# Performance work log

Measured on AMD Instinct MI355X. Metric: run time of the kernel, lower is better.

The kernel has to match this reference:

```python
import jax, jax.numpy as jnp
import numpy as np
import math

B, N, D = 128, 64, 2
H, M, L = 64, 64, 2
OMEGA = 1.0


def setup_inputs() -> dict:
    key = jax.random.key(0)
    ks = jax.random.split(key, 32)
    s = 0.1  # param scale
    rn = lambda k, shp: jax.random.normal(k, shp, dtype=jnp.float32) * s
    inp = {
        "x": jax.random.normal(ks[0], (B, N, D), dtype=jnp.float32),
        "spin": jnp.zeros((B, N, 1), jnp.float32),
        "node_w1": rn(ks[1], (D + 1, H)), "node_b1": rn(ks[2], (H,)),
        "node_w2": rn(ks[3], (H, H)), "node_b2": rn(ks[4], (H,)),
        "edge_w1": rn(ks[5], (D + 2, M)), "edge_b1": rn(ks[6], (M,)),
        "edge_w2": rn(ks[7], (M, M)), "edge_b2": rn(ks[8], (M,)),
        "v2e_w1": rn(ks[9], (L, H + M, M)), "v2e_b1": rn(ks[10], (L, M)),
        "v2e_w2": rn(ks[11], (L, M, M)), "v2e_b2": rn(ks[12], (L, M)),
        "e2v_w1": rn(ks[13], (L, M, H)), "e2v_b1": rn(ks[14], (L, H)),
        "e2v_w2": rn(ks[15], (L, H, H)), "e2v_b2": rn(ks[16], (L, H)),
        "head_w1": rn(ks[17], (H, H)), "head_b1": rn(ks[18], (H,)),
        "head_w2": rn(ks[19], (H, D)), "head_b2": rn(ks[20], (D,)),
        # bf_scale_init=0.3 -> softplus-inverse
        "scale": jnp.array([math.log(math.exp(0.3) - 1.0)], jnp.float32),
    }
    return inp


def _mlp(x, w1, b1, w2, b2, act):
    return act(x @ w1 + b1) @ w2 + b2


def reference(x, spin, node_w1, node_b1, node_w2, node_b2,
              edge_w1, edge_b1, edge_w2, edge_b2,
              v2e_w1, v2e_b1, v2e_w2, v2e_b2,
              e2v_w1, e2v_b1, e2v_w2, e2v_b2,
              head_w1, head_b1, head_w2, head_b2, scale):
    gelu = lambda t: jax.nn.gelu(t, approximate=False)  # torch exact GELU
    b, n, d = x.shape
    xs = x * jnp.float32(math.sqrt(OMEGA))
    # node embedding: [B,N,H]
    hv = _mlp(jnp.concatenate([xs, spin], -1), node_w1, node_b1, node_w2, node_b2, gelu)
    # dense pairwise edge features; dr[b,i,j] = xs[b,j] - xs[b,i]
    dr = xs[:, None, :, :] - xs[:, :, None, :]            # [B,N,N,D]
    r2 = jnp.sum(dr * dr, axis=-1, keepdims=True)          # [B,N,N,1]
    rr = jnp.sqrt(r2 + 1e-12)
    he = _mlp(jnp.concatenate([dr, rr, r2], -1), edge_w1, edge_b1, edge_w2, edge_b2, gelu)  # [B,N,N,M]
    # mask excludes self-edges (i==j) from aggregation (they were never created
    # in the original edge list; their dense entries never influence off-diag values)
    mask = (1.0 - jnp.eye(n, dtype=x.dtype))[None, :, :, None]
    inv = jnp.float32(1.0 / max(n - 1, 1))
    for l in range(v2e_w1.shape[0]):
        hvb = jnp.broadcast_to(hv[:, :, None, :], (b, n, n, hv.shape[-1]))  # source node i
        he = _mlp(jnp.concatenate([hvb, he], -1), v2e_w1[l], v2e_b1[l], v2e_w2[l], v2e_b2[l], gelu)
        m = _mlp(he, e2v_w1[l], e2v_b1[l], e2v_w2[l], e2v_b2[l], gelu)      # [B,N,N,H]
        hv = hv + jnp.sum(m * mask, axis=1) * inv           # scatter-add over sources i into j
    dx = _mlp(hv, head_w1, head_b1, head_w2, head_b2, jnp.tanh) * jax.nn.softplus(scale[0])
    return dx - jnp.mean(dx, axis=1, keepdims=True)
```

## Files before the change

kernel.cpp:

```cpp
#include <hip/hip_runtime.h>
#include <math.h>


typedef unsigned short u16;
typedef unsigned int u32;
typedef _Float16 half8 __attribute__((ext_vector_type(8)));
typedef __attribute__((ext_vector_type(4))) float floatx4;

#define TS 72
#define HROW 72
#define HBLK (64 * HROW)

__device__ __forceinline__ float gelu_f(float x) {
    float s = fabsf(x) * 0.70710678118654752f;
    float q = fmaf(fmaf(fmaf(fmaf(0.078108f, s, 0.000972f), s, 0.230389f), s, 0.278393f), s, 1.0f);
    float q2 = q * q;
    float r = __builtin_amdgcn_rcpf(q2 * q2);
    float t = 0.5f * x * r;
    return x > 0.f ? x - t : t;
}

__global__ __launch_bounds__(256) void k_preA(
    const float* __restrict__ ew2, const float* __restrict__ w1he0,
    const float* __restrict__ w2_0, const float* __restrict__ u1_0,
    const float* __restrict__ w1he1, const float* __restrict__ w2_1,
    const float* __restrict__ u1_1,
    const float* __restrict__ eb2, const float* __restrict__ b2_0,
    const float* __restrict__ c1_0, const float* __restrict__ b2_1,
    const float* __restrict__ c1_1,
    const float* __restrict__ b1_0v, const float* __restrict__ b1nv,
    const float* __restrict__ u2_0, const float* __restrict__ u2_1,
    const float* __restrict__ w1n, const float* __restrict__ hw1,
    _Float16* __restrict__ WF,
    float* __restrict__ biasB, float* __restrict__ biasC, float* __restrict__ biasD,
    float* __restrict__ pb0,
    float* __restrict__ u2_0T, float* __restrict__ u2_1T,
    float* __restrict__ w1nT, float* __restrict__ hw1T)
{
    int blk = blockIdx.x;
    if (blk < 64) {
        int s = blk >> 4;
        int idx = (blk & 15) * 256 + threadIdx.x;
        int k = idx >> 6, n = idx & 63;
        const float *A, *Bm;
        if (s == 0)      { A = ew2;  Bm = w1he0; }
        else if (s == 1) { A = w2_0; Bm = u1_0;  }
        else if (s == 2) { A = w2_0; Bm = w1he1; }
        else             { A = w2_1; Bm = u1_1;  }
        float acc = 0.f;
        for (int q = 0; q < 64; ++q) acc = fmaf(A[k * 64 + q], Bm[q * 64 + n], acc);
        int kc = k >> 5, qd = (k >> 3) & 3, jj = k & 7;
        WF[(((s * 2 + kc) * 64 + n) * 4 + qd) * 8 + jj] = (_Float16)acc;
    } else if (blk == 64) {
        int s = threadIdx.x >> 6, cc = threadIdx.x & 63;
        if (s == 0) {
            float acc = b1_0v[cc];
            for (int q = 0; q < 64; ++q) acc = fmaf(eb2[q], w1he0[q * 64 + cc], acc);
            pb0[cc] = acc;
        } else {
            const float *bv, *Bm, *add; float* dst;
            if (s == 1)      { bv = b2_0; Bm = u1_0;  add = c1_0; dst = biasB; }
            else if (s == 2) { bv = b2_0; Bm = w1he1; add = b1nv; dst = biasC; }
            else             { bv = b2_1; Bm = u1_1;  add = c1_1; dst = biasD; }
            float acc = add[cc];
            for (int q = 0; q < 64; ++q) acc = fmaf(bv[q], Bm[q * 64 + cc], acc);
            dst[cc] = acc;
        }
    } else {
        int idx = (blk - 65) * 256 + threadIdx.x;
        int s = idx >> 12, r = idx & 4095, m = r >> 6, tc = r & 63;
        const float* W = s == 0 ? u2_0 : s == 1 ? u2_1 : s == 2 ? w1n : hw1;
        float* WT      = s == 0 ? u2_0T : s == 1 ? u2_1T : s == 2 ? w1nT : hw1T;
        WT[tc * 64 + m] = W[m * 64 + tc];
    }
}

__global__ __launch_bounds__(256) void k_preB(
    const float* __restrict__ x, const float* __restrict__ spin,
    const float* __restrict__ nw1, const float* __restrict__ nb1,
    const float* __restrict__ nw2, const float* __restrict__ nb2,
    const float* __restrict__ w1_0,
    const float* __restrict__ pb0,
    float* __restrict__ hv, float* __restrict__ p0T)
{
    __shared__ float a[4][64];
    __shared__ float shv[4][64];
    int w = threadIdx.x >> 6, h = threadIdx.x & 63;
    int node = blockIdx.x * 4 + w;
    float2 xv = ((const float2*)x)[node];
    float sp = spin[node];
    float z = fmaf(xv.x, nw1[h], fmaf(xv.y, nw1[64 + h], fmaf(sp, nw1[128 + h], nb1[h])));
    a[w][h] = gelu_f(z);
    float acc = nb2[h];
    for (int k = 0; k < 64; ++k) acc = fmaf(a[w][k], nw2[k * 64 + h], acc);
    hv[node * 64 + h] = acc;
    shv[w][h] = acc;
    float pa = pb0[h];
    for (int k = 0; k < 64; ++k) pa = fmaf(shv[w][k], w1_0[k * 64 + h], pa);
    p0T[(node >> 6) * 4096 + h * 64 + (node & 63)] = pa;
}

__device__ __forceinline__ void mfma_acc(
    const _Float16* __restrict__ tA, const _Float16* __restrict__ WF,
    int stage, int c, int quad, int nn, floatx4 acc[4])
{
    int sA = ((nn >> 2) & 3) << 3;
    #pragma unroll
    for (int kc = 0; kc < 2; ++kc) {
        half8 bf = *(const half8*)(WF + (((stage * 2 + kc) * 64 + c) * 4 + quad) * 8);
        int k0 = (kc * 32 + quad * 8) ^ sA;
        #pragma unroll
        for (int mt = 0; mt < 4; ++mt) {
            half8 af = *(const half8*)(tA + (mt * 16 + nn) * TS + k0);
            acc[mt] = __builtin_amdgcn_mfma_f32_16x16x32_f16(af, bf, acc[mt], 0, 0, 0);
        }
    }
}

__device__ __forceinline__ void init_bias(floatx4 acc[4], float bc) {
    #pragma unroll
    for (int mt = 0; mt < 4; ++mt) acc[mt] = (floatx4){bc, bc, bc, bc};
}
__device__ __forceinline__ void init_pT(floatx4 acc[4], const float* __restrict__ pT,
                                        int base) {
    #pragma unroll
    for (int mt = 0; mt < 4; ++mt)
        acc[mt] = *(const floatx4*)(pT + base + mt * 16);
}

__global__ __launch_bounds__(256, 8) void k_L0(
    const float* __restrict__ x,
    const float* __restrict__ ew1, const float* __restrict__ eb1,
    const float* __restrict__ p0T,
    const float* __restrict__ biasB,
    const float* __restrict__ u2_0T, const float* __restrict__ c2_0,
    const _Float16* __restrict__ WF,
    const float* __restrict__ hv0, float* __restrict__ hv1,
    const float* __restrict__ w1nT, const float* __restrict__ biasC,
    float* __restrict__ p1T,
    u16* __restrict__ he0g)
{
    __shared__ __align__(16) _Float16 tA[64 * TS];
    __shared__ float sS[64];
    __shared__ float shv[64];
    __shared__ float sred[256];
    int t = threadIdx.x, L = t & 63;
    int w = __builtin_amdgcn_readfirstlane(t >> 6);
    int nn = L & 15, quad = L >> 4;
    int c = w * 16 + nn;
    int cw = c ^ (quad << 3);
    int b = blockIdx.x >> 6, j = blockIdx.x & 63;

    float2 xi = ((const float2*)x)[b * 64 + L];
    float2 xj = ((const float2*)x)[b * 64 + j];
    float d0 = xj.x - xi.x, d1 = xj.y - xi.y;
    float r2 = fmaf(d0, d0, d1 * d1);
    float rr = sqrtf(r2 + 1e-12f);
    int swL = ((L >> 2) & 3) << 3;

    #pragma unroll
    for (int mb = 0; mb < 2; ++mb) {
        int m0 = w * 16 + mb * 8;
        half8 h8;
        #pragma unroll
        for (int kk = 0; kk < 8; ++kk) {
            int m = m0 + kk;
            float z = fmaf(d0, ew1[m], fmaf(d1, ew1[64 + m],
                      fmaf(rr, ew1[128 + m], fmaf(r2, ew1[192 + m], eb1[m]))));
            h8[kk] = (_Float16)gelu_f(z);
        }
        *(half8*)(tA + L * TS + (m0 ^ swL)) = h8;
    }
    __syncthreads();

    floatx4 acc[4];
    init_pT(acc, p0T, b * 4096 + c * 64 + quad * 4);
    mfma_acc(tA, WF, 0, c, quad, nn, acc);
    __syncthreads();
    #pragma unroll
    for (int mt = 0; mt < 4; ++mt)
        #pragma unroll
        for (int r = 0; r < 4; ++r)
            tA[(mt * 16 + quad * 4 + r) * TS + cw] = (_Float16)gelu_f(acc[mt][r]);
    __syncthreads();
    {
        const float4* srcl = (const float4*)tA;
        float4* dst4 = (float4*)(he0g + (size_t)blockIdx.x * HBLK);
        dst4[t] = srcl[t];
        dst4[t + 256] = srcl[t + 256];
        if (t < 64) dst4[t + 512] = srcl[t + 512];
    }
    init_bias(acc, biasB[c]);
    mfma_acc(tA, WF, 1, c, quad, nn, acc);
    {
        float s = 0.f;
        #pragma unroll
        for (int mt = 0; mt < 4; ++mt)
            #pragma unroll
            for (int r = 0; r < 4; ++r) {
                int i = mt * 16 + quad * 4 + r;
                float g = gelu_f(acc[mt][r]);
                s += (i == j) ? 0.f : g;
            }
        s += __shfl_xor(s, 16);
        s += __shfl_xor(s, 32);
        if (quad == 0) sS[c] = s;
    }
    __syncthreads();
    {
        const float4* sv4 = (const float4*)(sS + w * 16);
        const float4* uv4 = (const float4*)(u2_0T + L * 64 + w * 16);
        float g = 0.f;
        #pragma unroll
        for (int m4 = 0; m4 < 4; ++m4) {
            float4 sv = sv4[m4], uv = uv4[m4];
            g = fmaf(sv.x, uv.x, fmaf(sv.y, uv.y, fmaf(sv.z, uv.z, fmaf(sv.w, uv.w, g))));
        }
        sred[w * 64 + L] = g;
    }
    __syncthreads();
    if (t < 64) {
        float g = sred[t] + sred[64 + t] + sred[128 + t] + sred[192 + t];
        int o = blockIdx.x * 64 + t;
        float hvv = hv0[o] + g * (1.0f / 63.0f) + c2_0[t];
        hv1[o] = hvv;
        shv[t] = hvv;
    }
    __syncthreads();
    {
        const float4* hv4 = (const float4*)(shv + w * 16);
        const float4* wv4 = (const float4*)(w1nT + L * 64 + w * 16);
        float pa = 0.f;
        #pragma unroll
        for (int m4 = 0; m4 < 4; ++m4) {
            float4 sv = hv4[m4], uv = wv4[m4];
            pa = fmaf(sv.x, uv.x, fmaf(sv.y, uv.y, fmaf(sv.z, uv.z, fmaf(sv.w, uv.w, pa))));
        }
        sred[w * 64 + L] = pa;
    }
    __syncthreads();
    if (t < 64)
        p1T[b * 4096 + t * 64 + j] = biasC[t] + sred[t] + sred[64 + t] + sred[128 + t] + sred[192 + t];
}

__global__ __launch_bounds__(256, 8) void k_L1(
    const u16* __restrict__ he0g,
    const float* __restrict__ p1T,
    const float* __restrict__ biasD,
    const float* __restrict__ u2_1T, const float* __restrict__ c2_1,
    const _Float16* __restrict__ WF,
    const float* __restrict__ hv1,
    const float* __restrict__ hw1T, const float* __restrict__ hb1,
    const float* __restrict__ hw2, const float* __restrict__ hb2,
    const float* __restrict__ scale, float* __restrict__ dx)
{
    __shared__ __align__(16) _Float16 tA[64 * TS];
    __shared__ float sS[64];
    __shared__ float shv[64];
    __shared__ float sred[256];
    int t = threadIdx.x, L = t & 63;
    int w = __builtin_amdgcn_readfirstlane(t >> 6);
    int nn = L & 15, quad = L >> 4;
    int c = w * 16 + nn;
    int cw = c ^ (quad << 3);
    int b = blockIdx.x >> 6, j = blockIdx.x & 63;

    {
        const float4* src = (const float4*)(he0g + (size_t)blockIdx.x * HBLK);
        float4* dstl = (float4*)tA;
        for (int q = t; q < (HBLK * 2 / 16); q += 256)
            dstl[q] = src[q];
    }
    __syncthreads();

    floatx4 acc[4];
    init_pT(acc, p1T, b * 4096 + c * 64 + quad * 4);
    mfma_acc(tA, WF, 2, c, quad, nn, acc);
    __syncthreads();
    #pragma unroll
    for (int mt = 0; mt < 4; ++mt)
        #pragma unroll
        for (int r = 0; r < 4; ++r)
            tA[(mt * 16 + quad * 4 + r) * TS + cw] = (_Float16)gelu_f(acc[mt][r]);
    __syncthreads();
    init_bias(acc, biasD[c]);
    mfma_acc(tA, WF, 3, c, quad, nn, acc);
    {
        float s = 0.f;
        #pragma unroll
        for (int mt = 0; mt < 4; ++mt)
            #pragma unroll
            for (int r = 0; r < 4; ++r) {
                int i = mt * 16 + quad * 4 + r;
                float g = gelu_f(acc[mt][r]);
                s += (i == j) ? 0.f : g;
            }
        s += __shfl_xor(s, 16);
        s += __shfl_xor(s, 32);
        if (quad == 0) sS[c] = s;
    }
    __syncthreads();
    {
        const float4* sv4 = (const float4*)(sS + w * 16);
        const float4* uv4 = (const float4*)(u2_1T + L * 64 + w * 16);
        float g = 0.f;
        #pragma unroll
        for (int m4 = 0; m4 < 4; ++m4) {
            float4 sv = sv4[m4], uv = uv4[m4];
            g = fmaf(sv.x, uv.x, fmaf(sv.y, uv.y, fmaf(sv.z, uv.z, fmaf(sv.w, uv.w, g))));
        }
        sred[w * 64 + L] = g;
    }
    __syncthreads();
    if (t < 64) {
        float g = sred[t] + sred[64 + t] + sred[128 + t] + sred[192 + t];
        float hv2 = hv1[blockIdx.x * 64 + t] + g * (1.0f / 63.0f) + c2_1[t];
        shv[t] = hv2;
    }
    __syncthreads();
    {
        const float4* hv4 = (const float4*)(shv + w * 16);
        const float4* wv4 = (const float4*)(hw1T + L * 64 + w * 16);
        float a = 0.f;
        #pragma unroll
        for (int m4 = 0; m4 < 4; ++m4) {
            float4 sv = hv4[m4], uv = wv4[m4];
            a = fmaf(sv.x, uv.x, fmaf(sv.y, uv.y, fmaf(sv.z, uv.z, fmaf(sv.w, uv.w, a))));
        }
        sred[w * 64 + L] = a;
    }
    __syncthreads();
    if (t < 64) {
        float a = hb1[t] + sred[t] + sred[64 + t] + sred[128 + t] + sred[192 + t];
        float t1 = tanhf(a);
        float dd0 = t1 * hw2[t * 2], dd1 = t1 * hw2[t * 2 + 1];
        #pragma unroll
        for (int off = 1; off <= 32; off <<= 1) { dd0 += __shfl_xor(dd0, off); dd1 += __shfl_xor(dd1, off); }
        if (t == 0) {
            float sp = log1pf(__expf(scale[0]));
            dx[blockIdx.x * 2 + 0] = (dd0 + hb2[0]) * sp;
            dx[blockIdx.x * 2 + 1] = (dd1 + hb2[1]) * sp;
        }
    }
}

__global__ __launch_bounds__(64) void k_mean(
    const float* __restrict__ dx, float* __restrict__ out)
{
    __shared__ float s0[64], s1[64];
    int b = blockIdx.x, j = threadIdx.x;
    float2 d = ((const float2*)dx)[b * 64 + j];
    s0[j] = d.x; s1[j] = d.y;
    __syncthreads();
    float m0 = 0.f, m1 = 0.f;
    for (int q = 0; q < 64; ++q) { m0 += s0[q]; m1 += s1[q]; }
    ((float2*)out)[b * 64 + j] = make_float2(d.x - m0 * (1.0f / 64.0f), d.y - m1 * (1.0f / 64.0f));
}

__global__ void k_beacon(float* out, float code) { out[0] = code; }

extern "C" void kernel_launch(void* const* d_in, const int* in_sizes, int n_in,
                              void* d_out, int out_size, void* d_ws, size_t ws_size,
                              hipStream_t stream)
{
    static const int exp_sizes[23] = {
        16384, 8192, 192, 64, 4096, 64,
        256, 64, 4096, 64,
        16384, 128, 8192, 128,
        8192, 128, 8192, 128,
        4096, 64, 128, 2, 1
    };
    float* hv0 = (float*)d_ws;
    float* hv1 = hv0 + 524288;
    float* p0T = hv1 + 524288;
    float* p1T = p0T + 524288;
    float* dx  = p1T + 524288;
    float* u2_0T = dx + 16384;
    float* u2_1T = u2_0T + 4096;
    float* w1nT  = u2_1T + 4096;
    float* hw1T  = w1nT + 4096;
    float* biasB = hw1T + 4096;
    float* biasC = biasB + 64;
    float* biasD = biasC + 64;
    float* pb0   = biasD + 64;
    _Float16* WF = (_Float16*)(pb0 + 64);
    u16* he0g  = (u16*)(WF + 16384);
    const size_t need = (size_t)((char*)(he0g + (size_t)8192 * HBLK) - (char*)d_ws);

    int bad = -1;
    if (n_in != 23 || out_size != 16384) bad = 98;
    else if (ws_size < need) bad = 97;
    else for (int i = 0; i < 23; ++i)
        if (in_sizes[i] != exp_sizes[i]) { bad = i; break; }
    if (bad >= 0) {
        k_beacon<<<1, 1, 0, stream>>>((float*)d_out, 2e6f + bad * 1e4f);
        return;
    }

    const float* x      = (const float*)d_in[0];
    const float* spin   = (const float*)d_in[1];
    const float* nw1    = (const float*)d_in[2];
    const float* nb1    = (const float*)d_in[3];
    const float* nw2    = (const float*)d_in[4];
    const float* nb2    = (const float*)d_in[5];
    const float* ew1    = (const float*)d_in[6];
    const float* eb1    = (const float*)d_in[7];
    const float* ew2    = (const float*)d_in[8];
    const float* eb2    = (const float*)d_in[9];
    const float* v2e_w1 = (const float*)d_in[10];
    const float* v2e_b1 = (const float*)d_in[11];
    const float* v2e_w2 = (const float*)d_in[12];
    const float* v2e_b2 = (const float*)d_in[13];
    const float* e2v_w1 = (const float*)d_in[14];
    const float* e2v_b1 = (const float*)d_in[15];
    const float* e2v_w2 = (const float*)d_in[16];
    const float* e2v_b2 = (const float*)d_in[17];
    const float* hw1    = (const float*)d_in[18];
    const float* hb1    = (const float*)d_in[19];
    const float* hw2    = (const float*)d_in[20];
    const float* hb2    = (const float*)d_in[21];
    const float* scale  = (const float*)d_in[22];

    k_preA<<<129, 256, 0, stream>>>(
        ew2, v2e_w1 + 4096, v2e_w2, e2v_w1,
        v2e_w1 + 12288, v2e_w2 + 4096, e2v_w1 + 4096,
        eb2, v2e_b2, e2v_b1, v2e_b2 + 64, e2v_b1 + 64,
        v2e_b1, v2e_b1 + 64,
        e2v_w2, e2v_w2 + 4096, v2e_w1 + 8192, hw1,
        WF, biasB, biasC, biasD, pb0,
        u2_0T, u2_1T, w1nT, hw1T);
    k_preB<<<2048, 256, 0, stream>>>(x, spin, nw1, nb1, nw2, nb2, v2e_w1, pb0, hv0, p0T);
    k_L0<<<8192, 256, 0, stream>>>(x, ew1, eb1,
        p0T, biasB, u2_0T, e2v_b2,
        WF, hv0, hv1,
        w1nT, biasC, p1T,
        he0g);
    k_L1<<<8192, 256, 0, stream>>>(he0g,
        p1T, biasD, u2_1T, e2v_b2 + 64,
        WF, hv1, hw1T, hb1, hw2, hb2, scale, dx);
    k_mean<<<128, 64, 0, stream>>>(dx, (float*)d_out);
}
```

Baseline: 240.3 us.

## Fold post-aggregation matvecs into precomposed weights, merge prep kernels, compact edge buffer

Precomputes composed matrices (u2_0·w1n1 and u2_1·hw1) so the per-node matvec after the scatter-add can be computed in parallel with the aggregation, removing a serial reduce/sync round in both layer kernels. The two preprocessing kernels are merged into one launch, and the node-side contribution pc0 is computed there. The intermediate edge buffer is stored unpadded (4096 halfs per block instead of 72-stride rows) with remapping on store/load, and a second LDS tile removes a barrier before overwriting. This adds extra LDS and a larger prep kernel, and the pc0 workspace.

```diff
diff --git a/kernel.cpp b/kernel.cpp
--- a/kernel.cpp
+++ b/kernel.cpp
@@ -8,8 +8,6 @@
 typedef __attribute__((ext_vector_type(4))) float floatx4;
 
 #define TS 72
-#define HROW 72
-#define HBLK (64 * HROW)
 
 __device__ __forceinline__ float gelu_f(float x) {
     float s = fabsf(x) * 0.70710678118654752f;
@@ -20,25 +18,32 @@
     return x > 0.f ? x - t : t;
 }
 
-__global__ __launch_bounds__(256) void k_preA(
+__global__ __launch_bounds__(256) void k_pre(
     const float* __restrict__ ew2, const float* __restrict__ w1he0,
     const float* __restrict__ w2_0, const float* __restrict__ u1_0,
     const float* __restrict__ w1he1, const float* __restrict__ w2_1,
     const float* __restrict__ u1_1,
+    const float* __restrict__ u2_0, const float* __restrict__ w1n1,
+    const float* __restrict__ u2_1, const float* __restrict__ hw1,
     const float* __restrict__ eb2, const float* __restrict__ b2_0,
     const float* __restrict__ c1_0, const float* __restrict__ b2_1,
     const float* __restrict__ c1_1,
     const float* __restrict__ b1_0v, const float* __restrict__ b1nv,
-    const float* __restrict__ u2_0, const float* __restrict__ u2_1,
-    const float* __restrict__ w1n, const float* __restrict__ hw1,
+    const float* __restrict__ hb1, const float* __restrict__ c2_1,
+    const float* __restrict__ c2_0,
+    const float* __restrict__ x, const float* __restrict__ spin,
+    const float* __restrict__ nw1, const float* __restrict__ nb1,
+    const float* __restrict__ nw2, const float* __restrict__ nb2,
+    const float* __restrict__ w1_0,
     _Float16* __restrict__ WF,
     float* __restrict__ biasB, float* __restrict__ biasC, float* __restrict__ biasD,
-    float* __restrict__ pb0,
-    float* __restrict__ u2_0T, float* __restrict__ u2_1T,
-    float* __restrict__ w1nT, float* __restrict__ hw1T)
+    float* __restrict__ hb1p,
+    float* __restrict__ u2_0T, float* __restrict__ hw1T,
+    float* __restrict__ UT, float* __restrict__ VT,
+    float* __restrict__ hv, float* __restrict__ p0T, float* __restrict__ pc0)
 {
     int blk = blockIdx.x;
-    if (blk < 64) {
+    if (blk < 96) {
         int s = blk >> 4;
         int idx = (blk & 15) * 256 + threadIdx.x;
         int k = idx >> 6, n = idx & 63;
@@ -46,17 +51,24 @@
         if (s == 0)      { A = ew2;  Bm = w1he0; }
         else if (s == 1) { A = w2_0; Bm = u1_0;  }
         else if (s == 2) { A = w2_0; Bm = w1he1; }
-        else             { A = w2_1; Bm = u1_1;  }
+        else if (s == 3) { A = w2_1; Bm = u1_1;  }
+        else if (s == 4) { A = u2_0; Bm = w1n1;  }
+        else             { A = u2_1; Bm = hw1;   }
         float acc = 0.f;
         for (int q = 0; q < 64; ++q) acc = fmaf(A[k * 64 + q], Bm[q * 64 + n], acc);
-        int kc = k >> 5, qd = (k >> 3) & 3, jj = k & 7;
-        WF[(((s * 2 + kc) * 64 + n) * 4 + qd) * 8 + jj] = (_Float16)acc;
-    } else if (blk == 64) {
+        if (s < 4) {
+            int kc = k >> 5, qd = (k >> 3) & 3, jj = k & 7;
+            WF[(((s * 2 + kc) * 64 + n) * 4 + qd) * 8 + jj] = (_Float16)acc;
+        } else {
+            float* T = (s == 4) ? UT : VT;
+            T[n * 64 + k] = acc;
+        }
+    } else if (blk == 96) {
         int s = threadIdx.x >> 6, cc = threadIdx.x & 63;
         if (s == 0) {
-            float acc = b1_0v[cc];
-            for (int q = 0; q < 64; ++q) acc = fmaf(eb2[q], w1he0[q * 64 + cc], acc);
-            pb0[cc] = acc;
+            float acc = hb1[cc];
+            for (int q = 0; q < 64; ++q) acc = fmaf(c2_1[q], hw1[q * 64 + cc], acc);
+            hb1p[cc] = acc;
         } else {
             const float *bv, *Bm, *add; float* dst;
             if (s == 1)      { bv = b2_0; Bm = u1_0;  add = c1_0; dst = biasB; }
@@ -66,38 +78,35 @@
             for (int q = 0; q < 64; ++q) acc = fmaf(bv[q], Bm[q * 64 + cc], acc);
             dst[cc] = acc;
         }
+    } else if (blk < 129) {
+        int idx = (blk - 97) * 256 + threadIdx.x;
+        int s = idx >> 12, r = idx & 4095, m = r >> 6, tc = r & 63;
+        const float* W = s == 0 ? u2_0 : hw1;
+        float* WT      = s == 0 ? u2_0T : hw1T;
+        WT[tc * 64 + m] = W[m * 64 + tc];
     } else {
-        int idx = (blk - 65) * 256 + threadIdx.x;
-        int s = idx >> 12, r = idx & 4095, m = r >> 6, tc = r & 63;
-        const float* W = s == 0 ? u2_0 : s == 1 ? u2_1 : s == 2 ? w1n : hw1;
-        float* WT      = s == 0 ? u2_0T : s == 1 ? u2_1T : s == 2 ? w1nT : hw1T;
-        WT[tc * 64 + m] = W[m * 64 + tc];
-    }
-}
-
-__global__ __launch_bounds__(256) void k_preB(
-    const float* __restrict__ x, const float* __restrict__ spin,
-    const float* __restrict__ nw1, const float* __restrict__ nb1,
-    const float* __restrict__ nw2, const float* __restrict__ nb2,
-    const float* __restrict__ w1_0,
-    const float* __restrict__ pb0,
-    float* __restrict__ hv, float* __restrict__ p0T)
-{
-    __shared__ float a[4][64];
-    __shared__ float shv[4][64];
-    int w = threadIdx.x >> 6, h = threadIdx.x & 63;
-    int node = blockIdx.x * 4 + w;
-    float2 xv = ((const float2*)x)[node];
-    float sp = spin[node];
-    float z = fmaf(xv.x, nw1[h], fmaf(xv.y, nw1[64 + h], fmaf(sp, nw1[128 + h], nb1[h])));
-    a[w][h] = gelu_f(z);
-    float acc = nb2[h];
-    for (int k = 0; k < 64; ++k) acc = fmaf(a[w][k], nw2[k * 64 + h], acc);
-    hv[node * 64 + h] = acc;
-    shv[w][h] = acc;
-    float pa = pb0[h];
-    for (int k = 0; k < 64; ++k) pa = fmaf(shv[w][k], w1_0[k * 64 + h], pa);
-    p0T[(node >> 6) * 4096 + h * 64 + (node & 63)] = pa;
+        __shared__ float a[4][64];
+        __shared__ float shv[4][64];
+        __shared__ float shvc[4][64];
+        int w = threadIdx.x >> 6, h = threadIdx.x & 63;
+        int node = (blk - 129) * 4 + w;
+        float2 xv = ((const float2*)x)[node];
+        float sp = spin[node];
+        float z = fmaf(xv.x, nw1[h], fmaf(xv.y, nw1[64 + h], fmaf(sp, nw1[128 + h], nb1[h])));
+        a[w][h] = gelu_f(z);
+        float acc = nb2[h];
+        for (int k = 0; k < 64; ++k) acc = fmaf(a[w][k], nw2[k * 64 + h], acc);
+        hv[node * 64 + h] = acc;
+        shv[w][h] = acc;
+        shvc[w][h] = acc + c2_0[h];
+        float pa = b1_0v[h];
+        for (int q = 0; q < 64; ++q) pa = fmaf(eb2[q], w1he0[q * 64 + h], pa);
+        for (int k = 0; k < 64; ++k) pa = fmaf(shv[w][k], w1_0[k * 64 + h], pa);
+        p0T[(node >> 6) * 4096 + h * 64 + (node & 63)] = pa;
+        float pc = 0.f;
+        for (int k = 0; k < 64; ++k) pc = fmaf(shvc[w][k], w1n1[k * 64 + h], pc);
+        pc0[node * 64 + h] = pc;
+    }
 }
 
 __device__ __forceinline__ void mfma_acc(
@@ -133,17 +142,18 @@
     const float* __restrict__ ew1, const float* __restrict__ eb1,
     const float* __restrict__ p0T,
     const float* __restrict__ biasB,
-    const float* __restrict__ u2_0T, const float* __restrict__ c2_0,
+    const float* __restrict__ u2_0T, const float* __restrict__ UT,
+    const float* __restrict__ c2_0,
+    const float* __restrict__ biasC, const float* __restrict__ pc0,
     const _Float16* __restrict__ WF,
     const float* __restrict__ hv0, float* __restrict__ hv1,
-    const float* __restrict__ w1nT, const float* __restrict__ biasC,
     float* __restrict__ p1T,
     u16* __restrict__ he0g)
 {
     __shared__ __align__(16) _Float16 tA[64 * TS];
+    __shared__ __align__(16) _Float16 tB[64 * TS];
     __shared__ float sS[64];
-    __shared__ float shv[64];
-    __shared__ float sred[256];
+    __shared__ float sredA[256], sredB[256];
     int t = threadIdx.x, L = t & 63;
     int w = __builtin_amdgcn_readfirstlane(t >> 6);
     int nn = L & 15, quad = L >> 4;
@@ -176,22 +186,21 @@
     floatx4 acc[4];
     init_pT(acc, p0T, b * 4096 + c * 64 + quad * 4);
     mfma_acc(tA, WF, 0, c, quad, nn, acc);
-    __syncthreads();
     #pragma unroll
     for (int mt = 0; mt < 4; ++mt)
         #pragma unroll
         for (int r = 0; r < 4; ++r)
-            tA[(mt * 16 + quad * 4 + r) * TS + cw] = (_Float16)gelu_f(acc[mt][r]);
-    __syncthreads();
-    {
-        const float4* srcl = (const float4*)tA;
-        float4* dst4 = (float4*)(he0g + (size_t)blockIdx.x * HBLK);
-        dst4[t] = srcl[t];
-        dst4[t + 256] = srcl[t + 256];
-        if (t < 64) dst4[t + 512] = srcl[t + 512];
+            tB[(mt * 16 + quad * 4 + r) * TS + cw] = (_Float16)gelu_f(acc[mt][r]);
+    __syncthreads();
+    {
+        const float4* srcl = (const float4*)tB;
+        float4* dst4 = (float4*)(he0g + (size_t)blockIdx.x * 4096);
+        int q0 = t, q1 = t + 256;
+        dst4[q0] = srcl[(q0 >> 3) * 9 + (q0 & 7)];
+        dst4[q1] = srcl[(q1 >> 3) * 9 + (q1 & 7)];
     }
     init_bias(acc, biasB[c]);
-    mfma_acc(tA, WF, 1, c, quad, nn, acc);
+    mfma_acc(tB, WF, 1, c, quad, nn, acc);
     {
         float s = 0.f;
         #pragma unroll
@@ -209,55 +218,43 @@
     __syncthreads();
     {
         const float4* sv4 = (const float4*)(sS + w * 16);
-        const float4* uv4 = (const float4*)(u2_0T + L * 64 + w * 16);
-        float g = 0.f;
+        const float4* uA4 = (const float4*)(u2_0T + L * 64 + w * 16);
+        const float4* uB4 = (const float4*)(UT + L * 64 + w * 16);
+        float dA = 0.f, dB = 0.f;
         #pragma unroll
         for (int m4 = 0; m4 < 4; ++m4) {
-            float4 sv = sv4[m4], uv = uv4[m4];
-            g = fmaf(sv.x, uv.x, fmaf(sv.y, uv.y, fmaf(sv.z, uv.z, fmaf(sv.w, uv.w, g))));
-        }
-        sred[w * 64 + L] = g;
+            float4 sv = sv4[m4], ua = uA4[m4], ub = uB4[m4];
+            dA = fmaf(sv.x, ua.x, fmaf(sv.y, ua.y, fmaf(sv.z, ua.z, fmaf(sv.w, ua.w, dA))));
+            dB = fmaf(sv.x, ub.x, fmaf(sv.y, ub.y, fmaf(sv.z, ub.z, fmaf(sv.w, ub.w, dB))));
+        }
+        sredA[w * 64 + L] = dA;
+        sredB[w * 64 + L] = dB;
     }
     __syncthreads();
     if (t < 64) {
-        float g = sred[t] + sred[64 + t] + sred[128 + t] + sred[192 + t];
+        float g = sredA[t] + sredA[64 + t] + sredA[128 + t] + sredA[192 + t];
         int o = blockIdx.x * 64 + t;
-        float hvv = hv0[o] + g * (1.0f / 63.0f) + c2_0[t];
-        hv1[o] = hvv;
-        shv[t] = hvv;
-    }
-    __syncthreads();
-    {
-        const float4* hv4 = (const float4*)(shv + w * 16);
-        const float4* wv4 = (const float4*)(w1nT + L * 64 + w * 16);
-        float pa = 0.f;
-        #pragma unroll
-        for (int m4 = 0; m4 < 4; ++m4) {
-            float4 sv = hv4[m4], uv = wv4[m4];
-            pa = fmaf(sv.x, uv.x, fmaf(sv.y, uv.y, fmaf(sv.z, uv.z, fmaf(sv.w, uv.w, pa))));
-        }
-        sred[w * 64 + L] = pa;
-    }
-    __syncthreads();
-    if (t < 64)
-        p1T[b * 4096 + t * 64 + j] = biasC[t] + sred[t] + sred[64 + t] + sred[128 + t] + sred[192 + t];
+        hv1[o] = hv0[o] + g * (1.0f / 63.0f) + c2_0[t];
+        float pb = sredB[t] + sredB[64 + t] + sredB[128 + t] + sredB[192 + t];
+        p1T[b * 4096 + t * 64 + j] = biasC[t] + pc0[o] + pb * (1.0f / 63.0f);
+    }
 }
 
 __global__ __launch_bounds__(256, 8) void k_L1(
     const u16* __restrict__ he0g,
     const float* __restrict__ p1T,
     const float* __restrict__ biasD,
-    const float* __restrict__ u2_1T, const float* __restrict__ c2_1,
+    const float* __restrict__ VT,
     const _Float16* __restrict__ WF,
     const float* __restrict__ hv1,
-    const float* __restrict__ hw1T, const float* __restrict__ hb1,
+    const float* __restrict__ hw1T, const float* __restrict__ hb1p,
     const float* __restrict__ hw2, const float* __restrict__ hb2,
     const float* __restrict__ scale, float* __restrict__ dx)
 {
     __shared__ __align__(16) _Float16 tA[64 * TS];
+    __shared__ __align__(16) _Float16 tB[64 * TS];
     __shared__ float sS[64];
-    __shared__ float shv[64];
-    __shared__ float sred[256];
+    __shared__ float sredA[256], sredB[256];
     int t = threadIdx.x, L = t & 63;
     int w = __builtin_amdgcn_readfirstlane(t >> 6);
     int nn = L & 15, quad = L >> 4;
@@ -266,25 +263,35 @@
     int b = blockIdx.x >> 6, j = blockIdx.x & 63;
 
     {
-        const float4* src = (const float4*)(he0g + (size_t)blockIdx.x * HBLK);
+        const float4* src = (const float4*)(he0g + (size_t)blockIdx.x * 4096);
         float4* dstl = (float4*)tA;
-        for (int q = t; q < (HBLK * 2 / 16); q += 256)
-            dstl[q] = src[q];
+        int q0 = t, q1 = t + 256;
+        dstl[(q0 >> 3) * 9 + (q0 & 7)] = src[q0];
+        dstl[(q1 >> 3) * 9 + (q1 & 7)] = src[q1];
+    }
+    float dA = 0.f;
+    {
+        const float4* hv4 = (const float4*)(hv1 + blockIdx.x * 64 + w * 16);
+        const float4* wv4 = (const float4*)(hw1T + L * 64 + w * 16);
+        #pragma unroll
+        for (int m4 = 0; m4 < 4; ++m4) {
+            float4 sv = hv4[m4], uv = wv4[m4];
+            dA = fmaf(sv.x, uv.x, fmaf(sv.y, uv.y, fmaf(sv.z, uv.z, fmaf(sv.w, uv.w, dA))));
+        }
     }
     __syncthreads();
 
     floatx4 acc[4];
     init_pT(acc, p1T, b * 4096 + c * 64 + quad * 4);
     mfma_acc(tA, WF, 2, c, quad, nn, acc);
-    __syncthreads();
     #pragma unroll
     for (int mt = 0; mt < 4; ++mt)
         #pragma unroll
         for (int r = 0; r < 4; ++r)
-            tA[(mt * 16 + quad * 4 + r) * TS + cw] = (_Float16)gelu_f(acc[mt][r]);
+            tB[(mt * 16 + quad * 4 + r) * TS + cw] = (_Float16)gelu_f(acc[mt][r]);
     __syncthreads();
     init_bias(acc, biasD[c]);
-    mfma_acc(tA, WF, 3, c, quad, nn, acc);
+    mfma_acc(tB, WF, 3, c, quad, nn, acc);
     {
         float s = 0.f;
         #pragma unroll
@@ -302,36 +309,21 @@
     __syncthreads();
     {
         const float4* sv4 = (const float4*)(sS + w * 16);
-        const float4* uv4 = (const float4*)(u2_1T + L * 64 + w * 16);
-        float g = 0.f;
+        const float4* uv4 = (const float4*)(VT + L * 64 + w * 16);
+        float dB = 0.f;
         #pragma unroll
         for (int m4 = 0; m4 < 4; ++m4) {
             float4 sv = sv4[m4], uv = uv4[m4];
-            g = fmaf(sv.x, uv.x, fmaf(sv.y, uv.y, fmaf(sv.z, uv.z, fmaf(sv.w, uv.w, g))));
-        }
-        sred[w * 64 + L] = g;
+            dB = fmaf(sv.x, uv.x, fmaf(sv.y, uv.y, fmaf(sv.z, uv.z, fmaf(sv.w, uv.w, dB))));
+        }
+        sredA[w * 64 + L] = dA;
+        sredB[w * 64 + L] = dB;
     }
     __syncthreads();
     if (t < 64) {
-        float g = sred[t] + sred[64 + t] + sred[128 + t] + sred[192 + t];
-        float hv2 = hv1[blockIdx.x * 64 + t] + g * (1.0f / 63.0f) + c2_1[t];
-        shv[t] = hv2;
-    }
-    __syncthreads();
-    {
-        const float4* hv4 = (const float4*)(shv + w * 16);
-        const float4* wv4 = (const float4*)(hw1T + L * 64 + w * 16);
-        float a = 0.f;
-        #pragma unroll
-        for (int m4 = 0; m4 < 4; ++m4) {
-            float4 sv = hv4[m4], uv = wv4[m4];
-            a = fmaf(sv.x, uv.x, fmaf(sv.y, uv.y, fmaf(sv.z, uv.z, fmaf(sv.w, uv.w, a))));
-        }
-        sred[w * 64 + L] = a;
-    }
-    __syncthreads();
-    if (t < 64) {
-        float a = hb1[t] + sred[t] + sred[64 + t] + sred[128 + t] + sred[192 + t];
+        float a = hb1p[t]
+                + sredA[t] + sredA[64 + t] + sredA[128 + t] + sredA[192 + t]
+                + (sredB[t] + sredB[64 + t] + sredB[128 + t] + sredB[192 + t]) * (1.0f / 63.0f);
         float t1 = tanhf(a);
         float dd0 = t1 * hw2[t * 2], dd1 = t1 * hw2[t * 2 + 1];
         #pragma unroll
@@ -374,18 +366,19 @@
     float* hv1 = hv0 + 524288;
     float* p0T = hv1 + 524288;
     float* p1T = p0T + 524288;
-    float* dx  = p1T + 524288;
+    float* pc0 = p1T + 524288;
+    float* dx  = pc0 + 524288;
     float* u2_0T = dx + 16384;
-    float* u2_1T = u2_0T + 4096;
-    float* w1nT  = u2_1T + 4096;
-    float* hw1T  = w1nT + 4096;
-    float* biasB = hw1T + 4096;
+    float* hw1T  = u2_0T + 4096;
+    float* UT    = hw1T + 4096;
+    float* VT    = UT + 4096;
+    float* biasB = VT + 4096;
     float* biasC = biasB + 64;
     float* biasD = biasC + 64;
-    float* pb0   = biasD + 64;
-    _Float16* WF = (_Float16*)(pb0 + 64);
+    float* hb1p  = biasD + 64;
+    _Float16* WF = (_Float16*)(hb1p + 64);
     u16* he0g  = (u16*)(WF + 16384);
-    const size_t need = (size_t)((char*)(he0g + (size_t)8192 * HBLK) - (char*)d_ws);
+    const size_t need = (size_t)((char*)(he0g + (size_t)8192 * 4096) - (char*)d_ws);
 
     int bad = -1;
     if (n_in != 23 || out_size != 16384) bad = 98;
@@ -421,22 +414,23 @@
     const float* hb2    = (const float*)d_in[21];
     const float* scale  = (const float*)d_in[22];
 
-    k_preA<<<129, 256, 0, stream>>>(
+    k_pre<<<2177, 256, 0, stream>>>(
         ew2, v2e_w1 + 4096, v2e_w2, e2v_w1,
         v2e_w1 + 12288, v2e_w2 + 4096, e2v_w1 + 4096,
+        e2v_w2, v2e_w1 + 8192, e2v_w2 + 4096, hw1,
         eb2, v2e_b2, e2v_b1, v2e_b2 + 64, e2v_b1 + 64,
         v2e_b1, v2e_b1 + 64,
-        e2v_w2, e2v_w2 + 4096, v2e_w1 + 8192, hw1,
-        WF, biasB, biasC, biasD, pb0,
-        u2_0T, u2_1T, w1nT, hw1T);
-    k_preB<<<2048, 256, 0, stream>>>(x, spin, nw1, nb1, nw2, nb2, v2e_w1, pb0, hv0, p0T);
+        hb1, e2v_b2 + 64, e2v_b2,
+        x, spin, nw1, nb1, nw2, nb2, v2e_w1,
+        WF, biasB, biasC, biasD, hb1p,
+        u2_0T, hw1T, UT, VT,
+        hv0, p0T, pc0);
     k_L0<<<8192, 256, 0, stream>>>(x, ew1, eb1,
-        p0T, biasB, u2_0T, e2v_b2,
-        WF, hv0, hv1,
-        w1nT, biasC, p1T,
+        p0T, biasB, u2_0T, UT, e2v_b2, biasC, pc0,
+        WF, hv0, hv1, p1T,
         he0g);
     k_L1<<<8192, 256, 0, stream>>>(he0g,
-        p1T, biasD, u2_1T, e2v_b2 + 64,
-        WF, hv1, hw1T, hb1, hw2, hb2, scale, dx);
+        p1T, biasD, VT,
+        WF, hv1, hw1T, hb1p, hw2, hb2, scale, dx);
     k_mean<<<128, 64, 0, stream>>>(dx, (float*)d_out);
 }
```

Result: slower. 254.4 us (+5.9%).
